# Kernel tuning notes

Hardware: AMD Instinct MI355X
Metric: run time of the kernel (lower is better)

## Reference

```python
import jax, jax.numpy as jnp
import numpy as np

NUM_EMBEDDINGS = 512
EMBEDDING_DIM = 64


def setup_inputs() -> dict:
    key = jax.random.key(0)
    k1, k2 = jax.random.split(key)
    z_e = jax.random.normal(k1, (32, EMBEDDING_DIM, 64, 64), dtype=jnp.float32)
    lim = 1.0 / NUM_EMBEDDINGS
    codebook = jax.random.uniform(k2, (NUM_EMBEDDINGS, EMBEDDING_DIM),
                                  dtype=jnp.float32, minval=-lim, maxval=lim)
    return {"z_e": z_e, "codebook": codebook}


def reference(z_e, codebook):
    B, C, H, W = z_e.shape
    # [B,C,H,W] -> [N, C] with N = B*H*W (channels-last flatten)
    z_flat = jnp.transpose(z_e, (0, 2, 3, 1)).reshape(-1, C)
    # squared L2 distance via ||a||^2 + ||b||^2 - 2 a.b (same math, no NxKxC tensor)
    d = (jnp.sum(z_flat * z_flat, axis=1, keepdims=True)          # [N,1]
         + jnp.sum(codebook * codebook, axis=1)[None, :]           # [1,K]
         - 2.0 * jnp.einsum('nc,kc->nk', z_flat, codebook))        # [N,K]
    encoding_indices = jnp.argmin(d, axis=1)                       # [N] int
    z_q = codebook[encoding_indices].reshape(B, H, W, C)
    z_q = jnp.transpose(z_q, (0, 3, 1, 2))                         # [B,C,H,W]
    return z_q, encoding_indices
```

## Files before the change

### kernel.cpp

```cpp
#include <hip/hip_runtime.h>
#include <stdint.h>


#pragma clang fp contract(off)

#define KCODES 512
#define CDIM 64
#define HW 4096
#define ZQ_ELEMS 8388608

typedef float f2 __attribute__((ext_vector_type(2)));

static __device__ __forceinline__ f2 pk_fma_s(f2 a, uint64_t b, f2 c) {
    f2 d;
    asm("v_pk_fma_f32 %0, %1, %2, %3" : "=v"(d) : "v"(a), "s"(b), "v"(c));
    return d;
}
static __device__ __forceinline__ f2 pk_add(f2 a, f2 b) {
    f2 d;
    asm("v_pk_add_f32 %0, %1, %2" : "=v"(d) : "v"(a), "v"(b));
    return d;
}

static __device__ __forceinline__ float cnorm_row(const float* __restrict__ row) {
    float r[8];
    #pragma unroll
    for (int j = 0; j < 8; ++j) r[j] = row[j] * row[j];
    #pragma unroll
    for (int i = 8; i < 64; i += 8) {
        #pragma unroll
        for (int j = 0; j < 8; ++j) r[j] = r[j] + row[i + j] * row[i + j];
    }
    return ((r[0] + r[1]) + (r[2] + r[3])) + ((r[4] + r[5]) + (r[6] + r[7]));
}

__global__ void cnorm_kernel(const float* __restrict__ cb,
                             float* __restrict__ cnorm_out) {
    int k = (int)blockIdx.x * 256 + (int)threadIdx.x;
    if (k < KCODES) cnorm_out[k] = cnorm_row(cb + (size_t)k * CDIM);
}

__global__ __launch_bounds__(256)
__attribute__((amdgpu_waves_per_eu(4, 4)))
void vq_kernel(
    const float* __restrict__ z_e,
    const float* __restrict__ cb,
    const float* __restrict__ cnorm_g,
    float* __restrict__ out)
{
    __shared__ float cnorm[KCODES];
    __shared__ float dcand[4 * 64];
    __shared__ int   kcand[4 * 64];

    if (cnorm_g) {
        #pragma unroll
        for (int k = (int)threadIdx.x; k < KCODES; k += 256)
            cnorm[k] = cnorm_g[k];
    } else {
        for (int k = (int)threadIdx.x; k < KCODES; k += 256)
            cnorm[k] = cnorm_row(cb + (size_t)k * CDIM);
    }

    const int lane = (int)threadIdx.x & 63;
    const int g = __builtin_amdgcn_readfirstlane((int)threadIdx.x >> 6);
    const int n0 = (int)blockIdx.x * 64;
    const int b = n0 / HW;
    const int hw0 = n0 % HW;
    const float* zp = z_e + (size_t)b * CDIM * HW + hw0 + lane;

    f2 zz2[CDIM / 2];
    #pragma unroll
    for (int m = 0; m < CDIM / 2; ++m) {
        f2 t;
        t.x = zp[(size_t)(2 * m) * HW];
        t.y = zp[(size_t)(2 * m + 1) * HW];
        zz2[m] = t;
    }

    float sz;
    {
        f2 pr[4];
        #pragma unroll
        for (int t = 0; t < 4; ++t) pr[t] = zz2[t] * zz2[t];
        #pragma unroll
        for (int i = 8; i < 64; i += 8) {
            #pragma unroll
            for (int t = 0; t < 4; ++t) {
                f2 zt = zz2[(i + 2 * t) / 2];
                pr[t] = pr[t] + zt * zt;
            }
        }
        float s01 = pr[0].x + pr[0].y;
        float s23 = pr[1].x + pr[1].y;
        float s45 = pr[2].x + pr[2].y;
        float s67 = pr[3].x + pr[3].y;
        sz = (s01 + s23) + (s45 + s67);
    }

    __syncthreads();

    f2 zero; zero.x = 0.f; zero.y = 0.f;

    float best = 3.4e38f;
    int bk = 0;
    const int k0 = g * 128;

    #pragma unroll 2
    for (int i = 0; i < 128; ++i) {
        const int k = k0 + i;
        const float* ck = cb + k * CDIM;
        const uint64_t* cq = (const uint64_t*)(const void*)ck;

        f2 pv[8];
        #pragma unroll
        for (int j = 0; j < 8; ++j) {
            pv[j] = pk_fma_s(zz2[j], cq[j],
                      pk_fma_s(zz2[8 + j], cq[8 + j],
                        pk_fma_s(zz2[16 + j], cq[16 + j],
                          pk_fma_s(zz2[24 + j], cq[24 + j], zero))));
        }
        f2 pe0 = pk_add(pv[0], pv[4]), pe1 = pk_add(pv[1], pv[5]);
        f2 pe2 = pk_add(pv[2], pv[6]), pe3 = pk_add(pv[3], pv[7]);
        f2 pf0 = pk_add(pe0, pe2), pf1 = pk_add(pe1, pe3);
        f2 pt = pk_add(pf0, pf1);
        float dot = pt.x + pt.y;

        float A = sz + cnorm[k];
        float d = fmaf(dot, -2.f, A);

        if (d < best) { best = d; bk = k; }
    }

    dcand[g * 64 + lane] = best;
    kcand[g * 64 + lane] = bk;
    __syncthreads();

    float bd = dcand[lane];
    int bi = kcand[lane];
    #pragma unroll
    for (int gg = 1; gg < 4; ++gg) {
        float d2 = dcand[gg * 64 + lane];
        int   k2 = kcand[gg * 64 + lane];
        if (d2 < bd) { bd = d2; bi = k2; }
    }

    if (g == 0) out[ZQ_ELEMS + n0 + lane] = (float)bi;

    const float* row = cb + (size_t)bi * CDIM;
    float* op = out + (size_t)b * CDIM * HW + hw0 + lane;
    #pragma unroll
    for (int c = 0; c < 16; ++c) {
        const int ch = g * 16 + c;
        op[(size_t)ch * HW] = row[ch];
    }
}

extern "C" void kernel_launch(void* const* d_in, const int* in_sizes, int n_in,
                              void* d_out, int out_size, void* d_ws, size_t ws_size,
                              hipStream_t stream) {
    const float* z_e = (const float*)d_in[0];
    const float* cb  = (const float*)d_in[1];
    float* out = (float*)d_out;

    float* cnorm_ws = nullptr;
    if (ws_size >= KCODES * sizeof(float)) {
        cnorm_ws = (float*)d_ws;
        cnorm_kernel<<<dim3(2), dim3(256), 0, stream>>>(cb, cnorm_ws);
    }
    vq_kernel<<<dim3(2048), dim3(256), 0, stream>>>(z_e, cb, cnorm_ws, out);
}
```

Measured before the change: 210.3 us.

## Process two pixel columns per thread to reuse each codebook scalar load

Each block now handles 128 pixels instead of 64. Every thread keeps two z vectors in registers and computes distances for both against each codebook row, so the scalar codebook loads and LDS norm reads are shared across two dot products. The grid is halved and the waves-per-EU hint is relaxed to 3 to make room for the doubled register footprint. The cost is roughly 64 more VGPRs per thread, which lowers occupancy, and the 4096-pixel plane must stay divisible by 128.

Measured after the change: 200.5 us. 4.7% less time.

```diff
diff --git a/kernel.cpp b/kernel.cpp
--- a/kernel.cpp
+++ b/kernel.cpp
@@ -8,6 +8,7 @@
 #define CDIM 64
 #define HW 4096
 #define ZQ_ELEMS 8388608
+#define NPB 128
 
 typedef float f2 __attribute__((ext_vector_type(2)));
 
@@ -34,6 +35,25 @@
     return ((r[0] + r[1]) + (r[2] + r[3])) + ((r[4] + r[5]) + (r[6] + r[7]));
 }
 
+static __device__ __forceinline__ float znorm_pairwise(const f2* zz2) {
+    f2 pr[4];
+    #pragma unroll
+    for (int t = 0; t < 4; ++t) pr[t] = zz2[t] * zz2[t];
+    #pragma unroll
+    for (int i = 8; i < 64; i += 8) {
+        #pragma unroll
+        for (int t = 0; t < 4; ++t) {
+            f2 zt = zz2[(i + 2 * t) / 2];
+            pr[t] = pr[t] + zt * zt;
+        }
+    }
+    float s01 = pr[0].x + pr[0].y;
+    float s23 = pr[1].x + pr[1].y;
+    float s45 = pr[2].x + pr[2].y;
+    float s67 = pr[3].x + pr[3].y;
+    return (s01 + s23) + (s45 + s67);
+}
+
 __global__ void cnorm_kernel(const float* __restrict__ cb,
                              float* __restrict__ cnorm_out) {
     int k = (int)blockIdx.x * 256 + (int)threadIdx.x;
@@ -41,7 +61,7 @@
 }
 
 __global__ __launch_bounds__(256)
-__attribute__((amdgpu_waves_per_eu(4, 4)))
+__attribute__((amdgpu_waves_per_eu(3)))
 void vq_kernel(
     const float* __restrict__ z_e,
     const float* __restrict__ cb,
@@ -49,8 +69,9 @@
     float* __restrict__ out)
 {
     __shared__ float cnorm[KCODES];
-    __shared__ float dcand[4 * 64];
-    __shared__ int   kcand[4 * 64];
+    __shared__ float dcand[4 * NPB];
+    __shared__ int   kcand[4 * NPB];
+    __shared__ int   kbest[NPB];
 
     if (cnorm_g) {
         #pragma unroll
@@ -63,95 +84,116 @@
 
     const int lane = (int)threadIdx.x & 63;
     const int g = __builtin_amdgcn_readfirstlane((int)threadIdx.x >> 6);
-    const int n0 = (int)blockIdx.x * 64;
+    const int n0 = (int)blockIdx.x * NPB;
     const int b = n0 / HW;
     const int hw0 = n0 % HW;
-    const float* zp = z_e + (size_t)b * CDIM * HW + hw0 + lane;
-
-    f2 zz2[CDIM / 2];
+    const float* zpa = z_e + (size_t)b * CDIM * HW + hw0 + lane;
+    const float* zpb = zpa + 64;
+
+    f2 zza[CDIM / 2], zzb[CDIM / 2];
     #pragma unroll
     for (int m = 0; m < CDIM / 2; ++m) {
         f2 t;
-        t.x = zp[(size_t)(2 * m) * HW];
-        t.y = zp[(size_t)(2 * m + 1) * HW];
-        zz2[m] = t;
-    }
-
-    float sz;
-    {
-        f2 pr[4];
-        #pragma unroll
-        for (int t = 0; t < 4; ++t) pr[t] = zz2[t] * zz2[t];
-        #pragma unroll
-        for (int i = 8; i < 64; i += 8) {
-            #pragma unroll
-            for (int t = 0; t < 4; ++t) {
-                f2 zt = zz2[(i + 2 * t) / 2];
-                pr[t] = pr[t] + zt * zt;
-            }
-        }
-        float s01 = pr[0].x + pr[0].y;
-        float s23 = pr[1].x + pr[1].y;
-        float s45 = pr[2].x + pr[2].y;
-        float s67 = pr[3].x + pr[3].y;
-        sz = (s01 + s23) + (s45 + s67);
-    }
+        t.x = zpa[(size_t)(2 * m) * HW];
+        t.y = zpa[(size_t)(2 * m + 1) * HW];
+        zza[m] = t;
+    }
+    #pragma unroll
+    for (int m = 0; m < CDIM / 2; ++m) {
+        f2 t;
+        t.x = zpb[(size_t)(2 * m) * HW];
+        t.y = zpb[(size_t)(2 * m + 1) * HW];
+        zzb[m] = t;
+    }
+
+    const float sza = znorm_pairwise(zza);
+    const float szb = znorm_pairwise(zzb);
 
     __syncthreads();
 
     f2 zero; zero.x = 0.f; zero.y = 0.f;
 
-    float best = 3.4e38f;
-    int bk = 0;
+    float best_a = 3.4e38f, best_b = 3.4e38f;
+    int bk_a = 0, bk_b = 0;
     const int k0 = g * 128;
 
-    #pragma unroll 2
     for (int i = 0; i < 128; ++i) {
         const int k = k0 + i;
         const float* ck = cb + k * CDIM;
         const uint64_t* cq = (const uint64_t*)(const void*)ck;
-
-        f2 pv[8];
-        #pragma unroll
-        for (int j = 0; j < 8; ++j) {
-            pv[j] = pk_fma_s(zz2[j], cq[j],
-                      pk_fma_s(zz2[8 + j], cq[8 + j],
-                        pk_fma_s(zz2[16 + j], cq[16 + j],
-                          pk_fma_s(zz2[24 + j], cq[24 + j], zero))));
-        }
-        f2 pe0 = pk_add(pv[0], pv[4]), pe1 = pk_add(pv[1], pv[5]);
-        f2 pe2 = pk_add(pv[2], pv[6]), pe3 = pk_add(pv[3], pv[7]);
-        f2 pf0 = pk_add(pe0, pe2), pf1 = pk_add(pe1, pe3);
-        f2 pt = pk_add(pf0, pf1);
-        float dot = pt.x + pt.y;
-
-        float A = sz + cnorm[k];
-        float d = fmaf(dot, -2.f, A);
-
-        if (d < best) { best = d; bk = k; }
-    }
-
-    dcand[g * 64 + lane] = best;
-    kcand[g * 64 + lane] = bk;
+        const float A0 = cnorm[k];
+
+        {
+            f2 pv[8];
+            #pragma unroll
+            for (int j = 0; j < 8; ++j) {
+                pv[j] = pk_fma_s(zza[j], cq[j],
+                          pk_fma_s(zza[8 + j], cq[8 + j],
+                            pk_fma_s(zza[16 + j], cq[16 + j],
+                              pk_fma_s(zza[24 + j], cq[24 + j], zero))));
+            }
+            f2 pe0 = pk_add(pv[0], pv[4]), pe1 = pk_add(pv[1], pv[5]);
+            f2 pe2 = pk_add(pv[2], pv[6]), pe3 = pk_add(pv[3], pv[7]);
+            f2 pf0 = pk_add(pe0, pe2), pf1 = pk_add(pe1, pe3);
+            f2 pt = pk_add(pf0, pf1);
+            float dot = pt.x + pt.y;
+            float A = sza + A0;
+            float d = fmaf(dot, -2.f, A);
+            if (d < best_a) { best_a = d; bk_a = k; }
+        }
+
+        {
+            f2 pv[8];
+            #pragma unroll
+            for (int j = 0; j < 8; ++j) {
+                pv[j] = pk_fma_s(zzb[j], cq[j],
+                          pk_fma_s(zzb[8 + j], cq[8 + j],
+                            pk_fma_s(zzb[16 + j], cq[16 + j],
+                              pk_fma_s(zzb[24 + j], cq[24 + j], zero))));
+            }
+            f2 pe0 = pk_add(pv[0], pv[4]), pe1 = pk_add(pv[1], pv[5]);
+            f2 pe2 = pk_add(pv[2], pv[6]), pe3 = pk_add(pv[3], pv[7]);
+            f2 pf0 = pk_add(pe0, pe2), pf1 = pk_add(pe1, pe3);
+            f2 pt = pk_add(pf0, pf1);
+            float dot = pt.x + pt.y;
+            float A = szb + A0;
+            float d = fmaf(dot, -2.f, A);
+            if (d < best_b) { best_b = d; bk_b = k; }
+        }
+    }
+
+    dcand[g * NPB + lane]      = best_a;
+    kcand[g * NPB + lane]      = bk_a;
+    dcand[g * NPB + 64 + lane] = best_b;
+    kcand[g * NPB + 64 + lane] = bk_b;
     __syncthreads();
 
-    float bd = dcand[lane];
-    int bi = kcand[lane];
-    #pragma unroll
-    for (int gg = 1; gg < 4; ++gg) {
-        float d2 = dcand[gg * 64 + lane];
-        int   k2 = kcand[gg * 64 + lane];
-        if (d2 < bd) { bd = d2; bi = k2; }
-    }
-
-    if (g == 0) out[ZQ_ELEMS + n0 + lane] = (float)bi;
-
-    const float* row = cb + (size_t)bi * CDIM;
-    float* op = out + (size_t)b * CDIM * HW + hw0 + lane;
+    const int tid = (int)threadIdx.x;
+    if (tid < NPB) {
+        float bd = dcand[tid];
+        int bi = kcand[tid];
+        #pragma unroll
+        for (int gg = 1; gg < 4; ++gg) {
+            float d2 = dcand[gg * NPB + tid];
+            int   k2 = kcand[gg * NPB + tid];
+            if (d2 < bd) { bd = d2; bi = k2; }
+        }
+        out[ZQ_ELEMS + n0 + tid] = (float)bi;
+        kbest[tid] = bi;
+    }
+    __syncthreads();
+
+    const int bi_a = kbest[lane];
+    const int bi_b = kbest[64 + lane];
+    const float* rowa = cb + (size_t)bi_a * CDIM;
+    const float* rowb = cb + (size_t)bi_b * CDIM;
+    float* opa = out + (size_t)b * CDIM * HW + hw0 + lane;
+    float* opb = opa + 64;
     #pragma unroll
     for (int c = 0; c < 16; ++c) {
         const int ch = g * 16 + c;
-        op[(size_t)ch * HW] = row[ch];
+        opa[(size_t)ch * HW] = rowa[ch];
+        opb[(size_t)ch * HW] = rowb[ch];
     }
 }
 
@@ -167,5 +209,5 @@
         cnorm_ws = (float*)d_ws;
         cnorm_kernel<<<dim3(2), dim3(256), 0, stream>>>(cb, cnorm_ws);
     }
-    vq_kernel<<<dim3(2048), dim3(256), 0, stream>>>(z_e, cb, cnorm_ws, out);
-}
+    vq_kernel<<<dim3(131072 / NPB), dim3(256), 0, stream>>>(z_e, cb, cnorm_ws, out);
+}
```
